# Performance work log

Hardware: AMD Instinct MI355X
Metric: run time of the kernel (lower is better)

## Reference

```python
import jax, jax.numpy as jnp
import numpy as np

STEP = 0.1          # step_size
MAX_STEPS = 50      # max_steps
MAX_CURV = 100.0    # max_curvature
DX = 1.0            # grid_spacing
B, H, W, D = 2, 96, 96, 96


def _gradient(f):
    # central differences with replicate (edge) padding; f: (B,H,W,D)
    fp = jnp.pad(f, ((0, 0), (1, 1), (1, 1), (1, 1)), mode='edge')
    gx = (fp[:, 2:, 1:-1, 1:-1] - fp[:, :-2, 1:-1, 1:-1]) / (2 * DX)
    gy = (fp[:, 1:-1, 2:, 1:-1] - fp[:, 1:-1, :-2, 1:-1]) / (2 * DX)
    gz = (fp[:, 1:-1, 1:-1, 2:] - fp[:, 1:-1, 1:-1, :-2]) / (2 * DX)
    return jnp.stack([gx, gy, gz], axis=-1)  # (B,H,W,D,3)


def _christoffel(Phi):
    # Gamma^i_jk = d_ij g_k + d_ik g_j - d_jk g_i with g = grad(Phi)
    g = _gradient(Phi)                       # (B,H,W,D,3)
    I = jnp.eye(3, dtype=Phi.dtype)
    return (I[:, :, None] * g[..., None, None, :]
            + I[:, None, :] * g[..., None, :, None]
            - I[None, :, :] * g[..., :, None, None])  # (B,H,W,D,3,3,3)


def _accel(pos, vel, Gamma, dims_f, dims_i):
    # nearest-cell lookup of Gamma at normalized positions, then a^i = -G^i_jk v^j v^k
    idx = jnp.clip((pos * dims_f).astype(jnp.int32), 0, dims_i)  # (B,3)
    b = jnp.arange(pos.shape[0])
    G = Gamma[b, idx[:, 0], idx[:, 1], idx[:, 2]]  # (B,3,3,3)
    a = -jnp.einsum('bijk,bj,bk->bi', G, vel, vel)
    return jnp.clip(a, -MAX_CURV, MAX_CURV)


def _rk4_step(pos, vel, Gamma, dims_f, dims_i):
    h = STEP
    k1v = vel
    k1a = _accel(pos, vel, Gamma, dims_f, dims_i)
    k2v = vel + 0.5 * h * k1a
    k2a = _accel(pos + 0.5 * h * k1v, k2v, Gamma, dims_f, dims_i)
    k3v = vel + 0.5 * h * k2a
    k3a = _accel(pos + 0.5 * h * k2v, k3v, Gamma, dims_f, dims_i)
    k4v = vel + h * k3a
    k4a = _accel(pos + h * k3v, k4v, Gamma, dims_f, dims_i)
    pos_new = pos + (h / 6.0) * (k1v + 2 * k2v + 2 * k3v + k4v)
    vel_new = vel + (h / 6.0) * (k1a + 2 * k2a + 2 * k3a + k4a)
    return pos_new, vel_new


def setup_inputs() -> dict:
    key = jax.random.key(0)
    k1, k2, k3 = jax.random.split(key, 3)
    start_pos = jax.random.uniform(k1, (B, 3), dtype=jnp.float32)
    start_vel = jax.random.normal(k2, (B, 3), dtype=jnp.float32)
    Phi = jax.random.normal(k3, (B, H, W, D), dtype=jnp.float32)
    return {"start_pos": start_pos, "start_vel": start_vel, "Phi": Phi}


def reference(start_pos, start_vel, Phi):
    _, h, w, d = Phi.shape
    dims_f = jnp.array([h - 1, w - 1, d - 1], dtype=Phi.dtype)
    dims_i = jnp.array([h - 1, w - 1, d - 1], dtype=jnp.int32)
    Gamma = _christoffel(Phi)  # precomputed once, as in the original

    def step(carry, _):
        pos, vel = carry
        pos, vel = _rk4_step(pos, vel, Gamma, dims_f, dims_i)
        return (pos, vel), (pos, vel)

    _, (ps, vs) = jax.lax.scan(step, (start_pos, start_vel), None, length=MAX_STEPS - 1)
    positions = jnp.concatenate([start_pos[:, None, :], jnp.moveaxis(ps, 0, 1)], axis=1)
    velocities = jnp.concatenate([start_vel[:, None, :], jnp.moveaxis(vs, 0, 1)], axis=1)
    return positions, velocities  # each (B, MAX_STEPS, 3)
```

## Files before the change

kernel.cpp:

```cpp
#include <hip/hip_runtime.h>

#pragma clang fp contract(off)

namespace {

constexpr int HD    = 96;
constexpr int STRX  = HD * HD;
constexpr int VOL   = HD * HD * HD;
constexpr int NSTEPS = 50;
constexpr int DIMI  = HD - 1;
constexpr float DIMF = 95.0f;
constexpr float MAXC = 100.0f;

struct V3 { float x, y, z; };

__device__ __forceinline__ int clampi(int v) {
    return v < 0 ? 0 : (v > DIMI ? DIMI : v);
}

__device__ __forceinline__ void load_nb(const float* __restrict__ base,
                                        const V3 p, float nb[6]) {
    int x = clampi((int)(p.x * DIMF));
    int y = clampi((int)(p.y * DIMF));
    int z = clampi((int)(p.z * DIMF));
    int xp = x < DIMI ? x + 1 : DIMI, xm = x > 0 ? x - 1 : 0;
    int yp = y < DIMI ? y + 1 : DIMI, ym = y > 0 ? y - 1 : 0;
    int zp = z < DIMI ? z + 1 : DIMI, zm = z > 0 ? z - 1 : 0;
    int rowx = x * STRX;
    nb[0] = base[xp * STRX + y * HD + z];
    nb[1] = base[xm * STRX + y * HD + z];
    nb[2] = base[rowx + yp * HD + z];
    nb[3] = base[rowx + ym * HD + z];
    nb[4] = base[rowx + y * HD + zp];
    nb[5] = base[rowx + y * HD + zm];
}

__device__ __forceinline__ V3 accel_from(const float nb[6], const V3 v) {
    float gx = (nb[0] - nb[1]) * 0.5f;
    float gy = (nb[2] - nb[3]) * 0.5f;
    float gz = (nb[4] - nb[5]) * 0.5f;
    float gv = gx * v.x + gy * v.y + gz * v.z;
    float vv = v.x * v.x + v.y * v.y + v.z * v.z;
    V3 a;
    a.x = -(2.0f * v.x * gv - gx * vv);
    a.y = -(2.0f * v.y * gv - gy * vv);
    a.z = -(2.0f * v.z * gv - gz * vv);
    a.x = fminf(fmaxf(a.x, -MAXC), MAXC);
    a.y = fminf(fmaxf(a.y, -MAXC), MAXC);
    a.z = fminf(fmaxf(a.z, -MAXC), MAXC);
    return a;
}

__device__ __forceinline__ V3 axpy(const V3 a, float s, const V3 b) {
    V3 r; r.x = a.x + s * b.x; r.y = a.y + s * b.y; r.z = a.z + s * b.z;
    return r;
}

}

__global__ void __launch_bounds__(256)
geodesic_kernel(const float* __restrict__ sp, const float* __restrict__ sv,
                const float* __restrict__ Phi, float* __restrict__ out,
                int B) {
    if (blockIdx.x > 0) {
        int nblk = gridDim.x - 1;
        const float4* p4 = (const float4*)Phi;
        long total4 = (long)B * VOL / 4;
        float acc = 0.f;
        for (long i = (long)(blockIdx.x - 1) * blockDim.x + threadIdx.x;
             i < total4; i += (long)nblk * blockDim.x) {
            float4 v = p4[i];
            acc += v.x + v.y + v.z + v.w;
        }
        asm volatile("" :: "v"(acc));
        return;
    }

    int b = threadIdx.x;
    if (b >= B) return;

    const float H   = 0.1f;
    const float H05 = 0.5f * H;
    const float H6  = (float)(0.1 / 6.0);

    const float* __restrict__ base = Phi + (long)b * VOL;
    float* __restrict__ opos = out;
    float* __restrict__ ovel = out + (long)B * NSTEPS * 3;

    V3 pos = { sp[b * 3 + 0], sp[b * 3 + 1], sp[b * 3 + 2] };
    V3 vel = { sv[b * 3 + 0], sv[b * 3 + 1], sv[b * 3 + 2] };

    long o0 = (long)b * NSTEPS * 3;
    opos[o0 + 0] = pos.x; opos[o0 + 1] = pos.y; opos[o0 + 2] = pos.z;
    ovel[o0 + 0] = vel.x; ovel[o0 + 1] = vel.y; ovel[o0 + 2] = vel.z;

    for (int t = 1; t < NSTEPS; ++t) {
        V3 p1 = pos;
        V3 p2 = axpy(pos, H05, vel);
        float nb1[6], nb2[6];
        load_nb(base, p1, nb1);
        load_nb(base, p2, nb2);

        V3 k1a = accel_from(nb1, vel);
        V3 k2v = axpy(vel, H05, k1a);
        V3 k2a = accel_from(nb2, k2v);
        V3 k3v = axpy(vel, H05, k2a);

        V3 p3 = axpy(pos, H05, k2v);
        V3 p4 = axpy(pos, H, k3v);
        float nb3[6], nb4[6];
        load_nb(base, p3, nb3);
        load_nb(base, p4, nb4);

        V3 k3a = accel_from(nb3, k3v);
        V3 k4v = axpy(vel, H, k3a);
        V3 k4a = accel_from(nb4, k4v);

        V3 sv_;
        sv_.x = vel.x + 2.0f * k2v.x + 2.0f * k3v.x + k4v.x;
        sv_.y = vel.y + 2.0f * k2v.y + 2.0f * k3v.y + k4v.y;
        sv_.z = vel.z + 2.0f * k2v.z + 2.0f * k3v.z + k4v.z;
        V3 sa;
        sa.x = k1a.x + 2.0f * k2a.x + 2.0f * k3a.x + k4a.x;
        sa.y = k1a.y + 2.0f * k2a.y + 2.0f * k3a.y + k4a.y;
        sa.z = k1a.z + 2.0f * k2a.z + 2.0f * k3a.z + k4a.z;
        pos = axpy(pos, H6, sv_);
        vel = axpy(vel, H6, sa);

        long ot = (long)b * NSTEPS * 3 + (long)t * 3;
        opos[ot + 0] = pos.x; opos[ot + 1] = pos.y; opos[ot + 2] = pos.z;
        ovel[ot + 0] = vel.x; ovel[ot + 1] = vel.y; ovel[ot + 2] = vel.z;
    }
}

extern "C" void kernel_launch(void* const* d_in, const int* in_sizes, int n_in,
                              void* d_out, int out_size, void* d_ws, size_t ws_size,
                              hipStream_t stream) {
    const float* sp  = (const float*)d_in[0];
    const float* sv  = (const float*)d_in[1];
    const float* phi = (const float*)d_in[2];
    float* out = (float*)d_out;
    int B = in_sizes[0] / 3;

    geodesic_kernel<<<dim3(1 + 128), dim3(256), 0, stream>>>(sp, sv, phi, out, B);
}
```

Measured before the change: 110.1 us.

## Warm each batch's Phi volume into the L2 of the XCC running its walker

Each batch's serial RK4 walker now runs in its own block and publishes its XCC id through a workspace flag. Helper blocks poll those flags and prefetch slices of only the matching batch's Phi volume, so the warm data lands in the L2 that the walker's loads will hit. The walker also raises its wave priority. This adds spin-polling on uninitialized workspace, which could match stale tags from an earlier call, and helpers on other XCCs simply exit.

```diff
diff --git a/kernel.cpp b/kernel.cpp
--- a/kernel.cpp
+++ b/kernel.cpp
@@ -11,11 +11,34 @@
 constexpr int DIMI  = HD - 1;
 constexpr float DIMF = 95.0f;
 constexpr float MAXC = 100.0f;
+constexpr unsigned TAG = 0x5A5A0000u;
 
 struct V3 { float x, y, z; };
 
 __device__ __forceinline__ int clampi(int v) {
     return v < 0 ? 0 : (v > DIMI ? DIMI : v);
+}
+
+__device__ __forceinline__ int xcc_id() {
+    unsigned v;
+    asm volatile("s_getreg_b32 %0, hwreg(HW_REG_XCC_ID)" : "=s"(v));
+    return (int)(v & 0xFu);
+}
+
+__device__ __forceinline__ void warm_slice(const float* __restrict__ base,
+                                           int slice, int nslices,
+                                           int tid, int nthr) {
+    const float4* p4 = (const float4*)base;
+    int n4  = VOL / 4;
+    int per = (n4 + nslices - 1) / nslices;
+    int lo  = slice * per;
+    int hi  = lo + per; if (hi > n4) hi = n4;
+    float acc = 0.f;
+    for (int i = lo + tid; i < hi; i += nthr) {
+        float4 v = p4[i];
+        acc += v.x + v.y + v.z + v.w;
+    }
+    asm volatile("" :: "v"(acc));
 }
 
 __device__ __forceinline__ void load_nb(const float* __restrict__ base,
@@ -61,76 +84,104 @@
 __global__ void __launch_bounds__(256)
 geodesic_kernel(const float* __restrict__ sp, const float* __restrict__ sv,
                 const float* __restrict__ Phi, float* __restrict__ out,
-                int B) {
-    if (blockIdx.x > 0) {
-        int nblk = gridDim.x - 1;
-        const float4* p4 = (const float4*)Phi;
-        long total4 = (long)B * VOL / 4;
-        float acc = 0.f;
-        for (long i = (long)(blockIdx.x - 1) * blockDim.x + threadIdx.x;
-             i < total4; i += (long)nblk * blockDim.x) {
-            float4 v = p4[i];
-            acc += v.x + v.y + v.z + v.w;
+                int B, unsigned* __restrict__ ws) {
+    int xcc = xcc_id();
+
+    if (blockIdx.x < (unsigned)B) {
+        int b = blockIdx.x;
+        const float* __restrict__ base = Phi + (long)b * VOL;
+
+        if (threadIdx.x == 0) {
+            __hip_atomic_store(&ws[b], TAG | (unsigned)xcc,
+                               __ATOMIC_RELAXED, __HIP_MEMORY_SCOPE_AGENT);
         }
-        asm volatile("" :: "v"(acc));
+        if (threadIdx.x >= 64) {
+            warm_slice(base, 0, 16, threadIdx.x - 64, 192);
+            return;
+        }
+        if (threadIdx.x != 0) return;
+
+        __builtin_amdgcn_s_setprio(1);
+
+        const float H   = 0.1f;
+        const float H05 = 0.5f * H;
+        const float H6  = (float)(0.1 / 6.0);
+
+        float* __restrict__ opos = out;
+        float* __restrict__ ovel = out + (long)B * NSTEPS * 3;
+
+        V3 pos = { sp[b * 3 + 0], sp[b * 3 + 1], sp[b * 3 + 2] };
+        V3 vel = { sv[b * 3 + 0], sv[b * 3 + 1], sv[b * 3 + 2] };
+
+        long o0 = (long)b * NSTEPS * 3;
+        opos[o0 + 0] = pos.x; opos[o0 + 1] = pos.y; opos[o0 + 2] = pos.z;
+        ovel[o0 + 0] = vel.x; ovel[o0 + 1] = vel.y; ovel[o0 + 2] = vel.z;
+
+        for (int t = 1; t < NSTEPS; ++t) {
+            V3 p1 = pos;
+            V3 p2 = axpy(pos, H05, vel);
+            float nb1[6], nb2[6];
+            load_nb(base, p1, nb1);
+            load_nb(base, p2, nb2);
+
+            V3 k1a = accel_from(nb1, vel);
+            V3 k2v = axpy(vel, H05, k1a);
+            V3 k2a = accel_from(nb2, k2v);
+            V3 k3v = axpy(vel, H05, k2a);
+
+            V3 p3 = axpy(pos, H05, k2v);
+            V3 p4 = axpy(pos, H, k3v);
+            float nb3[6], nb4[6];
+            load_nb(base, p3, nb3);
+            load_nb(base, p4, nb4);
+
+            V3 k3a = accel_from(nb3, k3v);
+            V3 k4v = axpy(vel, H, k3a);
+            V3 k4a = accel_from(nb4, k4v);
+
+            V3 sv_;
+            sv_.x = vel.x + 2.0f * k2v.x + 2.0f * k3v.x + k4v.x;
+            sv_.y = vel.y + 2.0f * k2v.y + 2.0f * k3v.y + k4v.y;
+            sv_.z = vel.z + 2.0f * k2v.z + 2.0f * k3v.z + k4v.z;
+            V3 sa;
+            sa.x = k1a.x + 2.0f * k2a.x + 2.0f * k3a.x + k4a.x;
+            sa.y = k1a.y + 2.0f * k2a.y + 2.0f * k3a.y + k4a.y;
+            sa.z = k1a.z + 2.0f * k2a.z + 2.0f * k3a.z + k4a.z;
+            pos = axpy(pos, H6, sv_);
+            vel = axpy(vel, H6, sa);
+
+            long ot = (long)b * NSTEPS * 3 + (long)t * 3;
+            opos[ot + 0] = pos.x; opos[ot + 1] = pos.y; opos[ot + 2] = pos.z;
+            ovel[ot + 0] = vel.x; ovel[ot + 1] = vel.y; ovel[ot + 2] = vel.z;
+        }
         return;
     }
 
-    int b = threadIdx.x;
-    if (b >= B) return;
+    __shared__ int sh[2];
+    if (threadIdx.x == 0) {
+        int t0 = -1, t1 = -1;
+        for (int it = 0; it < 8192; ++it) {
+            unsigned a = __hip_atomic_load(&ws[0], __ATOMIC_RELAXED,
+                                           __HIP_MEMORY_SCOPE_AGENT);
+            unsigned c = __hip_atomic_load(&ws[1], __ATOMIC_RELAXED,
+                                           __HIP_MEMORY_SCOPE_AGENT);
+            if ((a & 0xFFFF0000u) == TAG) t0 = (int)(a & 0xFu);
+            if ((c & 0xFFFF0000u) == TAG) t1 = (int)(c & 0xFu);
+            if (t0 >= 0 && t1 >= 0) break;
+        }
+        sh[0] = t0; sh[1] = t1;
+    }
+    __syncthreads();
+    int t0 = sh[0], t1 = sh[1];
 
-    const float H   = 0.1f;
-    const float H05 = 0.5f * H;
-    const float H6  = (float)(0.1 / 6.0);
+    int batch = -1;
+    if (xcc == t0 && xcc == t1) batch = (int)(blockIdx.x & 1);
+    else if (xcc == t0) batch = 0;
+    else if (xcc == t1) batch = 1;
+    if (batch < 0) return;
 
-    const float* __restrict__ base = Phi + (long)b * VOL;
-    float* __restrict__ opos = out;
-    float* __restrict__ ovel = out + (long)B * NSTEPS * 3;
-
-    V3 pos = { sp[b * 3 + 0], sp[b * 3 + 1], sp[b * 3 + 2] };
-    V3 vel = { sv[b * 3 + 0], sv[b * 3 + 1], sv[b * 3 + 2] };
-
-    long o0 = (long)b * NSTEPS * 3;
-    opos[o0 + 0] = pos.x; opos[o0 + 1] = pos.y; opos[o0 + 2] = pos.z;
-    ovel[o0 + 0] = vel.x; ovel[o0 + 1] = vel.y; ovel[o0 + 2] = vel.z;
-
-    for (int t = 1; t < NSTEPS; ++t) {
-        V3 p1 = pos;
-        V3 p2 = axpy(pos, H05, vel);
-        float nb1[6], nb2[6];
-        load_nb(base, p1, nb1);
-        load_nb(base, p2, nb2);
-
-        V3 k1a = accel_from(nb1, vel);
-        V3 k2v = axpy(vel, H05, k1a);
-        V3 k2a = accel_from(nb2, k2v);
-        V3 k3v = axpy(vel, H05, k2a);
-
-        V3 p3 = axpy(pos, H05, k2v);
-        V3 p4 = axpy(pos, H, k3v);
-        float nb3[6], nb4[6];
-        load_nb(base, p3, nb3);
-        load_nb(base, p4, nb4);
-
-        V3 k3a = accel_from(nb3, k3v);
-        V3 k4v = axpy(vel, H, k3a);
-        V3 k4a = accel_from(nb4, k4v);
-
-        V3 sv_;
-        sv_.x = vel.x + 2.0f * k2v.x + 2.0f * k3v.x + k4v.x;
-        sv_.y = vel.y + 2.0f * k2v.y + 2.0f * k3v.y + k4v.y;
-        sv_.z = vel.z + 2.0f * k2v.z + 2.0f * k3v.z + k4v.z;
-        V3 sa;
-        sa.x = k1a.x + 2.0f * k2a.x + 2.0f * k3a.x + k4a.x;
-        sa.y = k1a.y + 2.0f * k2a.y + 2.0f * k3a.y + k4a.y;
-        sa.z = k1a.z + 2.0f * k2a.z + 2.0f * k3a.z + k4a.z;
-        pos = axpy(pos, H6, sv_);
-        vel = axpy(vel, H6, sa);
-
-        long ot = (long)b * NSTEPS * 3 + (long)t * 3;
-        opos[ot + 0] = pos.x; opos[ot + 1] = pos.y; opos[ot + 2] = pos.z;
-        ovel[ot + 0] = vel.x; ovel[ot + 1] = vel.y; ovel[ot + 2] = vel.z;
-    }
+    int slice = 1 + (int)((blockIdx.x >> 3) % 15);
+    warm_slice(Phi + (long)batch * VOL, slice, 16, threadIdx.x, 256);
 }
 
 extern "C" void kernel_launch(void* const* d_in, const int* in_sizes, int n_in,
@@ -140,7 +191,8 @@
     const float* sv  = (const float*)d_in[1];
     const float* phi = (const float*)d_in[2];
     float* out = (float*)d_out;
+    unsigned* ws = (unsigned*)d_ws;
     int B = in_sizes[0] / 3;
 
-    geodesic_kernel<<<dim3(1 + 128), dim3(256), 0, stream>>>(sp, sv, phi, out, B);
+    geodesic_kernel<<<dim3(B + 126), dim3(256), 0, stream>>>(sp, sv, phi, out, B, ws);
 }
```

After: 117.2 us. +6.5%, slower.
